# Performance work log

Hardware: AMD Instinct MI355X
Metric: run time of the kernel (lower is better)

## Reference

```python
import jax, jax.numpy as jnp
import numpy as np

D_MODEL = 1024
K_QUERY = 32
K_TOPK = 4

def setup_inputs() -> dict:
    key = jax.random.key(0)
    k1, k2, k3, k4, k5 = jax.random.split(key, 5)
    x = jax.random.normal(k1, (4, 2048, D_MODEL), dtype=jnp.float32)
    # nn.Linear(d_model, k_query): weight [k_query, d_model], bias [k_query]
    sc = 1.0 / np.sqrt(D_MODEL)
    Wq = jax.random.uniform(k2, (K_QUERY, D_MODEL), jnp.float32, -sc, sc)
    bq = jax.random.uniform(k3, (K_QUERY,), jnp.float32, -sc, sc)
    Wk = jax.random.uniform(k4, (K_QUERY, D_MODEL), jnp.float32, -sc, sc)
    bk = jax.random.uniform(k5, (K_QUERY,), jnp.float32, -sc, sc)
    return {"x": x, "Wq": Wq, "bq": bq, "Wk": Wk, "bk": bk}

def reference(x, Wq, bq, Wk, bk):
    # x: [B, T, D]
    queries = jnp.einsum('btd,kd->btk', x, Wq) + bq      # [B, T, Kq]
    keys = jnp.einsum('btd,kd->btk', x, Wk) + bk         # [B, T, Kq]
    sim = jnp.einsum('btk,bsk->bts', queries, keys)      # [B, T, T]
    sim = sim / jnp.sqrt(jnp.float32(queries.shape[-1]))
    _, topk_idx = jax.lax.top_k(sim, K_TOPK)              # [B, T, K]
    # gather neighbors per (b, t): x[b, topk_idx[b, t]] -> [B, T, K, D]
    neighbors = jax.vmap(lambda xb, ib: xb[ib])(x, topk_idx)
    gathered = neighbors.mean(axis=2)                     # [B, T, D]
    return gathered
```

## Files before the change

### kernel.cpp

```cpp
#include <hip/hip_runtime.h>
#include <math.h>

#define D_MODEL 1024
#define T_SEQ   2048
#define NBATCH  4
#define NROWS   (NBATCH * T_SEQ)
#define NOUT    64

#define T16F   1024

typedef float  v4f  __attribute__((ext_vector_type(4)));
typedef _Float16 v8hf __attribute__((ext_vector_type(8)));

__device__ __forceinline__ bool key_gt(float av, int ai, float bv, int bi) {
    return (av > bv) || (av == bv && ai < bi);
}

__device__ __forceinline__ void cmpswap(float& v0, int& i0, float& v1, int& i1) {
    bool sw = key_gt(v1, i1, v0, i0);
    float nv0 = sw ? v1 : v0, nv1 = sw ? v0 : v1;
    int   ni0 = sw ? i1 : i0, ni1 = sw ? i0 : i1;
    v0 = nv0; v1 = nv1; i0 = ni0; i1 = ni1;
}

__device__ __forceinline__ void merge4(float (&a)[4], int (&ai)[4],
                                       float b0, int j0, float b1, int j1,
                                       float b2, int j2, float b3, int j3) {
    if (!key_gt(a[0], ai[0], b3, j3)) { a[0] = b3; ai[0] = j3; }
    if (!key_gt(a[1], ai[1], b2, j2)) { a[1] = b2; ai[1] = j2; }
    if (!key_gt(a[2], ai[2], b1, j1)) { a[2] = b1; ai[2] = j1; }
    if (!key_gt(a[3], ai[3], b0, j0)) { a[3] = b0; ai[3] = j0; }
    cmpswap(a[0], ai[0], a[2], ai[2]);
    cmpswap(a[1], ai[1], a[3], ai[3]);
    cmpswap(a[0], ai[0], a[1], ai[1]);
    cmpswap(a[2], ai[2], a[3], ai[3]);
}

__device__ __forceinline__ void insert4(float (&tv)[4], int (&tix)[4], float v, int idx) {
    if (v > tv[3]) {
        bool g0 = v > tv[0], g1 = v > tv[1], g2 = v > tv[2];
        float n0 = g0 ? v : tv[0];
        int   m0 = g0 ? idx : tix[0];
        float n1 = g1 ? (g0 ? tv[0] : v) : tv[1];
        int   m1 = g1 ? (g0 ? tix[0] : idx) : tix[1];
        float n2 = g2 ? (g1 ? tv[1] : v) : tv[2];
        int   m2 = g2 ? (g1 ? tix[1] : idx) : tix[2];
        float n3 = g2 ? tv[2] : v;
        int   m3 = g2 ? tix[2] : idx;
        tv[0] = n0; tv[1] = n1; tv[2] = n2; tv[3] = n3;
        tix[0] = m0; tix[1] = m1; tix[2] = m2; tix[3] = m3;
    }
}

__device__ void run_probe16(int tid, int* __restrict__ tab)
{
    __shared__ _Float16 A16[16][32];
    __shared__ _Float16 B16[32][16];
    __shared__ float    D16[16][16];

    for (int e = tid; e < 512; e += 256) {
        const int m = e >> 5, k = e & 31;
        A16[m][k] = (_Float16)(float)(1 + (3 * m + 5 * k) % 61);
        const int kk = e >> 4, n = e & 15;
        B16[kk][n] = (_Float16)(float)(1 + (7 * kk + 11 * n) % 59);
    }
    __syncthreads();
    {
        const int m = tid >> 4, n = tid & 15;
        float s = 0.f;
        for (int k = 0; k < 32; ++k) s += (float)A16[m][k] * (float)B16[k][n];
        D16[m][n] = s;
    }
    __syncthreads();

    if (tid >= 64) return;
    const int lane = tid;

    v8hf a, b;
    const int ab = (lane >> 4) * 8;
    #pragma unroll
    for (int j = 0; j < 8; ++j) {
        a[j] = A16[lane & 15][ab + j];
        b[j] = B16[ab + j][lane & 15];
    }
    v4f c = {0.f, 0.f, 0.f, 0.f};
    c = __builtin_amdgcn_mfma_f32_16x16x32_f16(a, b, c, 0, 0, 0);

    bool ok0 = true;
    #pragma unroll
    for (int i = 0; i < 4; ++i)
        ok0 = ok0 && (c[i] == D16[4 * (lane >> 4) + i][lane & 15]);
    if (lane == 0) tab[T16F] = __all(ok0) ? 0 : -1;
}

__global__ __launch_bounds__(256) void wprep_probe(
    const float* __restrict__ x,
    const float* __restrict__ Wq, const float* __restrict__ Wk,
    double* __restrict__ Wdt, _Float16* __restrict__ Wh, _Float16* __restrict__ Wl,
    _Float16* __restrict__ Xh, _Float16* __restrict__ Xl, int do_xsplit,
    int* __restrict__ tab)
{
    const int tid = threadIdx.x;
    const int gid = blockIdx.x * 256 + tid;

    if (gid < 65536) {
        {
            const int o = gid & 63;
            const int d = gid >> 6;
            float v = (o < 32) ? Wq[(size_t)o * D_MODEL + d]
                               : Wk[(size_t)(o - 32) * D_MODEL + d];
            Wdt[(size_t)d * 64 + o] = (double)v;
        }
        {
            const int o = gid >> 10;
            const int d = gid & 1023;
            float v = (o < 32) ? Wq[(size_t)o * D_MODEL + d]
                               : Wk[(size_t)(o - 32) * D_MODEL + d];
            _Float16 h = (_Float16)v;
            Wh[(size_t)o * D_MODEL + d] = h;
            Wl[(size_t)o * D_MODEL + d] = (_Float16)(v - (float)h);
        }
    }

    if (do_xsplit) {
        #pragma unroll
        for (int j = 0; j < 8; ++j) {
            const size_t f4 = (size_t)j * 262144 + gid;
            float4 v = reinterpret_cast<const float4*>(x)[f4];
            const float f[4] = {v.x, v.y, v.z, v.w};
            union { _Float16 h[4]; short4 s; } uh, ul;
            #pragma unroll
            for (int e = 0; e < 4; ++e) {
                _Float16 h = (_Float16)f[e];
                uh.h[e] = h;
                ul.h[e] = (_Float16)(f[e] - (float)h);
            }
            reinterpret_cast<short4*>(Xh)[f4] = uh.s;
            reinterpret_cast<short4*>(Xl)[f4] = ul.s;
        }
    }

    if (blockIdx.x == 0) run_probe16(tid, tab);
}

__global__ __launch_bounds__(256, 4) void proj(
    const float* __restrict__ x, const double* __restrict__ Wdt,
    const _Float16* __restrict__ Wh, const _Float16* __restrict__ Wl,
    const _Float16* __restrict__ Xh, const _Float16* __restrict__ Xl, int use_xsplit,
    const float* __restrict__ bq, const float* __restrict__ bk_,
    const int* __restrict__ tab,
    float* __restrict__ Qt, float* __restrict__ Kt,
    _Float16* __restrict__ Qh, _Float16* __restrict__ Ql,
    _Float16* __restrict__ Kh, _Float16* __restrict__ Kl)
{
    const int tid  = threadIdx.x;
    const int lane = tid & 63;
    const int wav  = tid >> 6;
    const int og   = __builtin_amdgcn_readfirstlane(wav);
    const int row0 = blockIdx.x * 16;

    if (tab[T16F] == 0) {
        const int m  = lane & 15;
        const int ko = (lane >> 4) * 8;
        const _Float16* bH = Wh + (size_t)(og * 16 + m) * D_MODEL + ko;
        const _Float16* bL = Wl + (size_t)(og * 16 + m) * D_MODEL + ko;

        v4f hh = {0.f, 0.f, 0.f, 0.f};
        v4f hl = {0.f, 0.f, 0.f, 0.f};
        v4f lh = {0.f, 0.f, 0.f, 0.f};

        if (use_xsplit) {
            const _Float16* aH = Xh + (size_t)(row0 + m) * D_MODEL + ko;
            const _Float16* aL = Xl + (size_t)(row0 + m) * D_MODEL + ko;
            #pragma unroll 4
            for (int kc = 0; kc < 32; ++kc) {
                v8hf ah = *reinterpret_cast<const v8hf*>(aH + kc * 32);
                v8hf al = *reinterpret_cast<const v8hf*>(aL + kc * 32);
                v8hf bh = *reinterpret_cast<const v8hf*>(bH + kc * 32);
                v8hf bl = *reinterpret_cast<const v8hf*>(bL + kc * 32);
                hh = __builtin_amdgcn_mfma_f32_16x16x32_f16(ah, bh, hh, 0, 0, 0);
                hl = __builtin_amdgcn_mfma_f32_16x16x32_f16(ah, bl, hl, 0, 0, 0);
                lh = __builtin_amdgcn_mfma_f32_16x16x32_f16(al, bh, lh, 0, 0, 0);
            }
        } else {
            const float* xrow = x + (size_t)(row0 + m) * D_MODEL + ko;
            #pragma unroll 4
            for (int kc = 0; kc < 32; ++kc) {
                float4 x0 = *reinterpret_cast<const float4*>(xrow + kc * 32);
                float4 x1 = *reinterpret_cast<const float4*>(xrow + kc * 32 + 4);
                const float f[8] = {x0.x, x0.y, x0.z, x0.w, x1.x, x1.y, x1.z, x1.w};
                v8hf ah, al;
                #pragma unroll
                for (int e = 0; e < 8; ++e) {
                    _Float16 h = (_Float16)f[e];
                    ah[e] = h;
                    al[e] = (_Float16)(f[e] - (float)h);
                }
                v8hf bh = *reinterpret_cast<const v8hf*>(bH + kc * 32);
                v8hf bl = *reinterpret_cast<const v8hf*>(bL + kc * 32);
                hh = __builtin_amdgcn_mfma_f32_16x16x32_f16(ah, bh, hh, 0, 0, 0);
                hl = __builtin_amdgcn_mfma_f32_16x16x32_f16(ah, bl, hl, 0, 0, 0);
                lh = __builtin_amdgcn_mfma_f32_16x16x32_f16(al, bh, lh, 0, 0, 0);
            }
        }

        #pragma unroll
        for (int i = 0; i < 4; ++i) {
            const float t = (hh[i] + hl[i]) + lh[i];
            const int o   = og * 16 + m;
            const int row = row0 + 4 * (lane >> 4) + i;
            const float bias = (o < 32) ? bq[o] : bk_[o - 32];
            const float v = t + bias;
            const _Float16 h = (_Float16)v;
            const _Float16 l = (_Float16)(v - (float)h);
            if (o < 32) {
                Qh[(size_t)row * 32 + o] = h;
                Ql[(size_t)row * 32 + o] = l;
            } else {
                Kh[(size_t)row * 32 + (o - 32)] = h;
                Kl[(size_t)row * 32 + (o - 32)] = l;
            }
        }
        return;
    }

    {
        const int n  = lane & 15;
        const int r4 = (lane >> 4) * 4;
        const int o  = og * 16 + n;
        const double* wcol = Wdt + o;
        double acc[4] = {0.0, 0.0, 0.0, 0.0};
        for (int d = 0; d < D_MODEL; ++d) {
            double wv = wcol[(size_t)d * 64];
            #pragma unroll
            for (int i = 0; i < 4; ++i)
                acc[i] = fma((double)x[(size_t)(row0 + r4 + i) * D_MODEL + d], wv, acc[i]);
        }
        #pragma unroll
        for (int i = 0; i < 4; ++i) {
            const int row = row0 + r4 + i;
            const int bb  = row >> 11, tt = row & 2047;
            const double bias = (o < 32) ? (double)bq[o] : (double)bk_[o - 32];
            const float v = (float)(acc[i] + bias);
            if (o < 32) Qt[((size_t)bb * 32 + o) * T_SEQ + tt] = v;
            else        Kt[((size_t)bb * 32 + (o - 32)) * T_SEQ + tt] = v;
        }
    }
}

__global__ __launch_bounds__(512, 4) void sim_topk_gather(
    const float* __restrict__ x,
    const _Float16* __restrict__ Qh, const _Float16* __restrict__ Ql,
    const _Float16* __restrict__ Kh, const _Float16* __restrict__ Kl,
    const float* __restrict__ Qt, const float* __restrict__ Kt,
    const int* __restrict__ tab,
    float* __restrict__ out)
{
    __shared__ float sV[8][16][4];
    __shared__ int   sI[8][16][4];
    __shared__ float sVf[16][32][4];
    __shared__ int   sIf[16][32][4];
    __shared__ int   topIdx[16][4];

    const int tid  = threadIdx.x;
    const int lane = tid & 63;
    const int wav  = tid >> 6;
    const int tt   = blockIdx.x & 127;
    const int b    = blockIdx.x >> 7;
    const int row0g = b * T_SEQ + tt * 16;

    if (tab[T16F] == 0) {
        const int m  = lane & 15;
        const int ko = (lane >> 4) * 8;
        v8hf qh = *reinterpret_cast<const v8hf*>(Qh + (size_t)(row0g + m) * 32 + ko);
        v8hf ql = *reinterpret_cast<const v8hf*>(Ql + (size_t)(row0g + m) * 32 + ko);
        const _Float16* KhB = Kh + (size_t)b * T_SEQ * 32;
        const _Float16* KlB = Kl + (size_t)b * T_SEQ * 32;

        float tv[4]; int tix[4];
        #pragma unroll
        for (int j = 0; j < 4; ++j) { tv[j] = -INFINITY; tix[j] = 0x7fffffff; }

        const int sq = wav * 256;
        #pragma unroll 4
        for (int st = 0; st < 16; ++st) {
            const int s0 = sq + st * 16;
            v8hf kh = *reinterpret_cast<const v8hf*>(KhB + (size_t)(s0 + m) * 32 + ko);
            v8hf kl = *reinterpret_cast<const v8hf*>(KlB + (size_t)(s0 + m) * 32 + ko);
            v4f c = {0.f, 0.f, 0.f, 0.f};
            c = __builtin_amdgcn_mfma_f32_16x16x32_f16(kh, qh, c, 0, 0, 0);
            c = __builtin_amdgcn_mfma_f32_16x16x32_f16(kl, qh, c, 0, 0, 0);
            c = __builtin_amdgcn_mfma_f32_16x16x32_f16(kh, ql, c, 0, 0, 0);
            c = __builtin_amdgcn_mfma_f32_16x16x32_f16(kl, ql, c, 0, 0, 0);
            const int sb = s0 + 4 * (lane >> 4);
            #pragma unroll
            for (int i = 0; i < 4; ++i) insert4(tv, tix, c[i], sb + i);
        }

        #pragma unroll
        for (int mk = 16; mk <= 32; mk <<= 1) {
            float b0 = __shfl_xor(tv[0], mk, 64);
            float b1 = __shfl_xor(tv[1], mk, 64);
            float b2 = __shfl_xor(tv[2], mk, 64);
            float b3 = __shfl_xor(tv[3], mk, 64);
            int   j0 = __shfl_xor(tix[0], mk, 64);
            int   j1 = __shfl_xor(tix[1], mk, 64);
            int   j2 = __shfl_xor(tix[2], mk, 64);
            int   j3 = __shfl_xor(tix[3], mk, 64);
            merge4(tv, tix, b0, j0, b1, j1, b2, j2, b3, j3);
        }

        if (lane < 16) {
            #pragma unroll
            for (int j = 0; j < 4; ++j) {
                sV[wav][lane][j] = tv[j];
                sI[wav][lane][j] = tix[j];
            }
        }
        __syncthreads();

        if (tid < 16) {
            float mv[4]; int mi[4];
            #pragma unroll
            for (int j = 0; j < 4; ++j) { mv[j] = sV[0][tid][j]; mi[j] = sI[0][tid][j]; }
            #pragma unroll
            for (int w = 1; w < 8; ++w)
                merge4(mv, mi,
                       sV[w][tid][0], sI[w][tid][0],
                       sV[w][tid][1], sI[w][tid][1],
                       sV[w][tid][2], sI[w][tid][2],
                       sV[w][tid][3], sI[w][tid][3]);
            #pragma unroll
            for (int j = 0; j < 4; ++j) topIdx[tid][j] = mi[j];
        }
        __syncthreads();
    } else {
        const float* QtB = Qt + (size_t)b * 32 * T_SEQ;
        const float* KtB = Kt + (size_t)b * 32 * T_SEQ;
        const int row   = tid >> 5;
        const int chunk = tid & 31;
        const int trow  = tt * 16 + row;
        float q[32];
        #pragma unroll 8
        for (int i = 0; i < 32; ++i) q[i] = QtB[(size_t)i * T_SEQ + trow];
        float tv4[4]; int tix4[4];
        #pragma unroll
        for (int j = 0; j < 4; ++j) { tv4[j] = -INFINITY; tix4[j] = 0x7fffffff; }
        const int sbeg = chunk * 64;
        for (int s = sbeg; s < sbeg + 64; ++s) {
            float sum = 0.f;
            #pragma unroll 8
            for (int i = 0; i < 32; ++i)
                sum = fmaf(q[i], KtB[(size_t)i * T_SEQ + s], sum);
            insert4(tv4, tix4, sum, s);
        }
        #pragma unroll
        for (int j = 0; j < 4; ++j) { sVf[row][chunk][j] = tv4[j]; sIf[row][chunk][j] = tix4[j]; }
        __syncthreads();
        if (tid < 16) {
            float mv[4]; int mi[4];
            #pragma unroll
            for (int j = 0; j < 4; ++j) { mv[j] = sVf[tid][0][j]; mi[j] = sIf[tid][0][j]; }
            for (int cc = 1; cc < 32; ++cc)
                merge4(mv, mi,
                       sVf[tid][cc][0], sIf[tid][cc][0],
                       sVf[tid][cc][1], sIf[tid][cc][1],
                       sVf[tid][cc][2], sIf[tid][cc][2],
                       sVf[tid][cc][3], sIf[tid][cc][3]);
            #pragma unroll
            for (int j = 0; j < 4; ++j) topIdx[tid][j] = mi[j];
        }
        __syncthreads();
    }

    const float* xb = x + (size_t)b * T_SEQ * D_MODEL;
    float* ob = out + (size_t)row0g * D_MODEL;
    const int rh = tid >> 8;
    const int t4 = tid & 255;
    #pragma unroll 2
    for (int rp = 0; rp < 8; ++rp) {
        const int r = rp * 2 + rh;
        const int i0 = topIdx[r][0], i1 = topIdx[r][1], i2 = topIdx[r][2], i3 = topIdx[r][3];
        float4 a0 = *(reinterpret_cast<const float4*>(xb + (size_t)i0 * D_MODEL) + t4);
        float4 a1 = *(reinterpret_cast<const float4*>(xb + (size_t)i1 * D_MODEL) + t4);
        float4 a2 = *(reinterpret_cast<const float4*>(xb + (size_t)i2 * D_MODEL) + t4);
        float4 a3 = *(reinterpret_cast<const float4*>(xb + (size_t)i3 * D_MODEL) + t4);
        float4 o;
        o.x = (a0.x + a1.x + a2.x + a3.x) * 0.25f;
        o.y = (a0.y + a1.y + a2.y + a3.y) * 0.25f;
        o.z = (a0.z + a1.z + a2.z + a3.z) * 0.25f;
        o.w = (a0.w + a1.w + a2.w + a3.w) * 0.25f;
        *(reinterpret_cast<float4*>(ob + (size_t)r * D_MODEL) + t4) = o;
    }
}

extern "C" void kernel_launch(void* const* d_in, const int* in_sizes, int n_in,
                              void* d_out, int out_size, void* d_ws, size_t ws_size,
                              hipStream_t stream) {
    const float* x  = (const float*)d_in[0];
    const float* Wq = (const float*)d_in[1];
    const float* bq = (const float*)d_in[2];
    const float* Wk = (const float*)d_in[3];
    const float* bk = (const float*)d_in[4];
    float* out = (float*)d_out;

    char* wsb = (char*)d_ws;
    int*      tab = (int*)wsb;
    double*   Wdt = (double*)(wsb + 8192);
    _Float16* Wh  = (_Float16*)(wsb + 8192 + 524288);
    _Float16* Wl  = (_Float16*)(wsb + 8192 + 524288 + 131072);
    float*    Qt  = (float*)(wsb + 8192 + 524288 + 262144);
    float*    Kt  = Qt + (size_t)NBATCH * 32 * T_SEQ;
    _Float16* Qh  = (_Float16*)((char*)Kt + (size_t)NBATCH * 32 * T_SEQ * 4);
    _Float16* Ql  = Qh + (size_t)NROWS * 32;
    _Float16* Kh  = Ql + (size_t)NROWS * 32;
    _Float16* Kl  = Kh + (size_t)NROWS * 32;
    _Float16* Xh  = Kl + (size_t)NROWS * 32;
    _Float16* Xl  = Xh + (size_t)NROWS * D_MODEL;

    const size_t need = 4988928 + 2 * (size_t)NROWS * D_MODEL * 2;
    const int use_xsplit = (ws_size >= need) ? 1 : 0;

    wprep_probe<<<dim3(1024), dim3(256), 0, stream>>>(x, Wq, Wk, Wdt, Wh, Wl,
                                                      Xh, Xl, use_xsplit, tab);
    proj<<<dim3(NROWS / 16), dim3(256), 0, stream>>>(x, Wdt, Wh, Wl, Xh, Xl, use_xsplit,
                                                     bq, bk, tab, Qt, Kt, Qh, Ql, Kh, Kl);
    sim_topk_gather<<<dim3(512), dim3(512), 0, stream>>>(x, Qh, Ql, Kh, Kl, Qt, Kt, tab, out);
}
```

Measured before the change: 160.2 us.

## Fuse weight/x fp16 splitting into projection, split-K across 16 waves, widen sim kernel

```diff
diff --git a/kernel.cpp b/kernel.cpp
--- a/kernel.cpp
+++ b/kernel.cpp
@@ -52,186 +52,143 @@
     }
 }
 
-__device__ void run_probe16(int tid, int* __restrict__ tab)
+__device__ int run_probe16_block(int tid, int nthr, int* __restrict__ tab, int wr)
 {
     __shared__ _Float16 A16[16][32];
     __shared__ _Float16 B16[32][16];
     __shared__ float    D16[16][16];
-
-    for (int e = tid; e < 512; e += 256) {
+    __shared__ int      flagS;
+
+    for (int e = tid; e < 512; e += nthr) {
         const int m = e >> 5, k = e & 31;
         A16[m][k] = (_Float16)(float)(1 + (3 * m + 5 * k) % 61);
         const int kk = e >> 4, n = e & 15;
         B16[kk][n] = (_Float16)(float)(1 + (7 * kk + 11 * n) % 59);
     }
     __syncthreads();
-    {
-        const int m = tid >> 4, n = tid & 15;
+    for (int e = tid; e < 256; e += nthr) {
+        const int m = e >> 4, n = e & 15;
         float s = 0.f;
         for (int k = 0; k < 32; ++k) s += (float)A16[m][k] * (float)B16[k][n];
         D16[m][n] = s;
     }
     __syncthreads();
 
-    if (tid >= 64) return;
-    const int lane = tid;
-
-    v8hf a, b;
-    const int ab = (lane >> 4) * 8;
-    #pragma unroll
-    for (int j = 0; j < 8; ++j) {
-        a[j] = A16[lane & 15][ab + j];
-        b[j] = B16[ab + j][lane & 15];
-    }
-    v4f c = {0.f, 0.f, 0.f, 0.f};
-    c = __builtin_amdgcn_mfma_f32_16x16x32_f16(a, b, c, 0, 0, 0);
-
-    bool ok0 = true;
-    #pragma unroll
-    for (int i = 0; i < 4; ++i)
-        ok0 = ok0 && (c[i] == D16[4 * (lane >> 4) + i][lane & 15]);
-    if (lane == 0) tab[T16F] = __all(ok0) ? 0 : -1;
-}
-
-__global__ __launch_bounds__(256) void wprep_probe(
+    if (tid < 64) {
+        const int lane = tid;
+        v8hf a, b;
+        const int ab = (lane >> 4) * 8;
+        #pragma unroll
+        for (int j = 0; j < 8; ++j) {
+            a[j] = A16[lane & 15][ab + j];
+            b[j] = B16[ab + j][lane & 15];
+        }
+        v4f c = {0.f, 0.f, 0.f, 0.f};
+        c = __builtin_amdgcn_mfma_f32_16x16x32_f16(a, b, c, 0, 0, 0);
+        bool ok0 = true;
+        #pragma unroll
+        for (int i = 0; i < 4; ++i)
+            ok0 = ok0 && (c[i] == D16[4 * (lane >> 4) + i][lane & 15]);
+        int found = __all(ok0) ? 0 : -1;
+        if (lane == 0) { flagS = found; if (wr) tab[T16F] = found; }
+    }
+    __syncthreads();
+    return flagS;
+}
+
+__global__ __launch_bounds__(1024, 8) void proj_fused(
     const float* __restrict__ x,
     const float* __restrict__ Wq, const float* __restrict__ Wk,
-    double* __restrict__ Wdt, _Float16* __restrict__ Wh, _Float16* __restrict__ Wl,
-    _Float16* __restrict__ Xh, _Float16* __restrict__ Xl, int do_xsplit,
-    int* __restrict__ tab)
-{
-    const int tid = threadIdx.x;
-    const int gid = blockIdx.x * 256 + tid;
-
-    if (gid < 65536) {
-        {
-            const int o = gid & 63;
-            const int d = gid >> 6;
-            float v = (o < 32) ? Wq[(size_t)o * D_MODEL + d]
-                               : Wk[(size_t)(o - 32) * D_MODEL + d];
-            Wdt[(size_t)d * 64 + o] = (double)v;
-        }
-        {
-            const int o = gid >> 10;
-            const int d = gid & 1023;
-            float v = (o < 32) ? Wq[(size_t)o * D_MODEL + d]
-                               : Wk[(size_t)(o - 32) * D_MODEL + d];
-            _Float16 h = (_Float16)v;
-            Wh[(size_t)o * D_MODEL + d] = h;
-            Wl[(size_t)o * D_MODEL + d] = (_Float16)(v - (float)h);
-        }
-    }
-
-    if (do_xsplit) {
-        #pragma unroll
-        for (int j = 0; j < 8; ++j) {
-            const size_t f4 = (size_t)j * 262144 + gid;
-            float4 v = reinterpret_cast<const float4*>(x)[f4];
-            const float f[4] = {v.x, v.y, v.z, v.w};
-            union { _Float16 h[4]; short4 s; } uh, ul;
-            #pragma unroll
-            for (int e = 0; e < 4; ++e) {
-                _Float16 h = (_Float16)f[e];
-                uh.h[e] = h;
-                ul.h[e] = (_Float16)(f[e] - (float)h);
-            }
-            reinterpret_cast<short4*>(Xh)[f4] = uh.s;
-            reinterpret_cast<short4*>(Xl)[f4] = ul.s;
-        }
-    }
-
-    if (blockIdx.x == 0) run_probe16(tid, tab);
-}
-
-__global__ __launch_bounds__(256, 4) void proj(
-    const float* __restrict__ x, const double* __restrict__ Wdt,
-    const _Float16* __restrict__ Wh, const _Float16* __restrict__ Wl,
-    const _Float16* __restrict__ Xh, const _Float16* __restrict__ Xl, int use_xsplit,
     const float* __restrict__ bq, const float* __restrict__ bk_,
-    const int* __restrict__ tab,
+    int* __restrict__ tab,
     float* __restrict__ Qt, float* __restrict__ Kt,
     _Float16* __restrict__ Qh, _Float16* __restrict__ Ql,
     _Float16* __restrict__ Kh, _Float16* __restrict__ Kl)
 {
+    __shared__ float comb[3][4][64][4];
+
     const int tid  = threadIdx.x;
     const int lane = tid & 63;
     const int wav  = tid >> 6;
-    const int og   = __builtin_amdgcn_readfirstlane(wav);
+    const int og   = __builtin_amdgcn_readfirstlane(wav & 3);
+    const int kq   = __builtin_amdgcn_readfirstlane(wav >> 2);
     const int row0 = blockIdx.x * 16;
 
-    if (tab[T16F] == 0) {
+    const int flag = run_probe16_block(tid, 1024, tab, blockIdx.x == 0);
+
+    if (flag == 0) {
         const int m  = lane & 15;
         const int ko = (lane >> 4) * 8;
-        const _Float16* bH = Wh + (size_t)(og * 16 + m) * D_MODEL + ko;
-        const _Float16* bL = Wl + (size_t)(og * 16 + m) * D_MODEL + ko;
+        const int kb = kq * 256;
+        const int o  = og * 16 + m;
+        const float* xrow = x + (size_t)(row0 + m) * D_MODEL + kb + ko;
+        const float* wrow = ((o < 32) ? Wq + (size_t)o * D_MODEL
+                                      : Wk + (size_t)(o - 32) * D_MODEL) + kb + ko;
 
         v4f hh = {0.f, 0.f, 0.f, 0.f};
         v4f hl = {0.f, 0.f, 0.f, 0.f};
         v4f lh = {0.f, 0.f, 0.f, 0.f};
-
-        if (use_xsplit) {
-            const _Float16* aH = Xh + (size_t)(row0 + m) * D_MODEL + ko;
-            const _Float16* aL = Xl + (size_t)(row0 + m) * D_MODEL + ko;
-            #pragma unroll 4
-            for (int kc = 0; kc < 32; ++kc) {
-                v8hf ah = *reinterpret_cast<const v8hf*>(aH + kc * 32);
-                v8hf al = *reinterpret_cast<const v8hf*>(aL + kc * 32);
-                v8hf bh = *reinterpret_cast<const v8hf*>(bH + kc * 32);
-                v8hf bl = *reinterpret_cast<const v8hf*>(bL + kc * 32);
-                hh = __builtin_amdgcn_mfma_f32_16x16x32_f16(ah, bh, hh, 0, 0, 0);
-                hl = __builtin_amdgcn_mfma_f32_16x16x32_f16(ah, bl, hl, 0, 0, 0);
-                lh = __builtin_amdgcn_mfma_f32_16x16x32_f16(al, bh, lh, 0, 0, 0);
+        #pragma unroll 2
+        for (int kc = 0; kc < 8; ++kc) {
+            float4 x0 = *reinterpret_cast<const float4*>(xrow + kc * 32);
+            float4 x1 = *reinterpret_cast<const float4*>(xrow + kc * 32 + 4);
+            float4 w0 = *reinterpret_cast<const float4*>(wrow + kc * 32);
+            float4 w1 = *reinterpret_cast<const float4*>(wrow + kc * 32 + 4);
+            const float xf[8] = {x0.x, x0.y, x0.z, x0.w, x1.x, x1.y, x1.z, x1.w};
+            const float wf[8] = {w0.x, w0.y, w0.z, w0.w, w1.x, w1.y, w1.z, w1.w};
+            v8hf ah, al, bh, bl;
+            #pragma unroll
+            for (int e = 0; e < 8; ++e) {
+                _Float16 h = (_Float16)xf[e];
+                ah[e] = h; al[e] = (_Float16)(xf[e] - (float)h);
+                _Float16 g = (_Float16)wf[e];
+                bh[e] = g; bl[e] = (_Float16)(wf[e] - (float)g);
             }
-        } else {
-            const float* xrow = x + (size_t)(row0 + m) * D_MODEL + ko;
-            #pragma unroll 4
-            for (int kc = 0; kc < 32; ++kc) {
-                float4 x0 = *reinterpret_cast<const float4*>(xrow + kc * 32);
-                float4 x1 = *reinterpret_cast<const float4*>(xrow + kc * 32 + 4);
-                const float f[8] = {x0.x, x0.y, x0.z, x0.w, x1.x, x1.y, x1.z, x1.w};
-                v8hf ah, al;
-                #pragma unroll
-                for (int e = 0; e < 8; ++e) {
-                    _Float16 h = (_Float16)f[e];
-                    ah[e] = h;
-                    al[e] = (_Float16)(f[e] - (float)h);
+            hh = __builtin_amdgcn_mfma_f32_16x16x32_f16(ah, bh, hh, 0, 0, 0);
+            hl = __builtin_amdgcn_mfma_f32_16x16x32_f16(ah, bl, hl, 0, 0, 0);
+            lh = __builtin_amdgcn_mfma_f32_16x16x32_f16(al, bh, lh, 0, 0, 0);
+        }
+
+        v4f t;
+        #pragma unroll
+        for (int i = 0; i < 4; ++i) t[i] = (hh[i] + hl[i]) + lh[i];
+
+        if (kq > 0) {
+            #pragma unroll
+            for (int i = 0; i < 4; ++i) comb[kq - 1][og][lane][i] = t[i];
+        }
+        __syncthreads();
+        if (kq == 0) {
+            #pragma unroll
+            for (int i = 0; i < 4; ++i) {
+                const float tot = (t[i] + comb[0][og][lane][i])
+                                + (comb[1][og][lane][i] + comb[2][og][lane][i]);
+                const int row = row0 + 4 * (lane >> 4) + i;
+                const float bias = (o < 32) ? bq[o] : bk_[o - 32];
+                const float v = tot + bias;
+                const _Float16 h = (_Float16)v;
+                const _Float16 l = (_Float16)(v - (float)h);
+                if (o < 32) {
+                    Qh[(size_t)row * 32 + o] = h;
+                    Ql[(size_t)row * 32 + o] = l;
+                } else {
+                    Kh[(size_t)row * 32 + (o - 32)] = h;
+                    Kl[(size_t)row * 32 + (o - 32)] = l;
                 }
-                v8hf bh = *reinterpret_cast<const v8hf*>(bH + kc * 32);
-                v8hf bl = *reinterpret_cast<const v8hf*>(bL + kc * 32);
-                hh = __builtin_amdgcn_mfma_f32_16x16x32_f16(ah, bh, hh, 0, 0, 0);
-                hl = __builtin_amdgcn_mfma_f32_16x16x32_f16(ah, bl, hl, 0, 0, 0);
-                lh = __builtin_amdgcn_mfma_f32_16x16x32_f16(al, bh, lh, 0, 0, 0);
             }
         }
-
-        #pragma unroll
-        for (int i = 0; i < 4; ++i) {
-            const float t = (hh[i] + hl[i]) + lh[i];
-            const int o   = og * 16 + m;
-            const int row = row0 + 4 * (lane >> 4) + i;
-            const float bias = (o < 32) ? bq[o] : bk_[o - 32];
-            const float v = t + bias;
-            const _Float16 h = (_Float16)v;
-            const _Float16 l = (_Float16)(v - (float)h);
-            if (o < 32) {
-                Qh[(size_t)row * 32 + o] = h;
-                Ql[(size_t)row * 32 + o] = l;
-            } else {
-                Kh[(size_t)row * 32 + (o - 32)] = h;
-                Kl[(size_t)row * 32 + (o - 32)] = l;
-            }
-        }
         return;
     }
 
-    {
+    if (kq == 0) {
         const int n  = lane & 15;
         const int r4 = (lane >> 4) * 4;
         const int o  = og * 16 + n;
-        const double* wcol = Wdt + o;
+        const float* wr = (o < 32) ? Wq + (size_t)o * D_MODEL
+                                   : Wk + (size_t)(o - 32) * D_MODEL;
         double acc[4] = {0.0, 0.0, 0.0, 0.0};
         for (int d = 0; d < D_MODEL; ++d) {
-            double wv = wcol[(size_t)d * 64];
+            const double wv = (double)wr[d];
             #pragma unroll
             for (int i = 0; i < 4; ++i)
                 acc[i] = fma((double)x[(size_t)(row0 + r4 + i) * D_MODEL + d], wv, acc[i]);
@@ -248,7 +205,7 @@
     }
 }
 
-__global__ __launch_bounds__(512, 4) void sim_topk_gather(
+__global__ __launch_bounds__(1024, 8) void sim_topk_gather(
     const float* __restrict__ x,
     const _Float16* __restrict__ Qh, const _Float16* __restrict__ Ql,
     const _Float16* __restrict__ Kh, const _Float16* __restrict__ Kl,
@@ -256,10 +213,10 @@
     const int* __restrict__ tab,
     float* __restrict__ out)
 {
-    __shared__ float sV[8][16][4];
-    __shared__ int   sI[8][16][4];
-    __shared__ float sVf[16][32][4];
-    __shared__ int   sIf[16][32][4];
+    __shared__ float sV[16][16][4];
+    __shared__ int   sI[16][16][4];
+    __shared__ float sVf[16][64][4];
+    __shared__ int   sIf[16][64][4];
     __shared__ int   topIdx[16][4];
 
     const int tid  = threadIdx.x;
@@ -281,9 +238,9 @@
         #pragma unroll
         for (int j = 0; j < 4; ++j) { tv[j] = -INFINITY; tix[j] = 0x7fffffff; }
 
-        const int sq = wav * 256;
-        #pragma unroll 4
-        for (int st = 0; st < 16; ++st) {
+        const int sq = wav * 128;
+        #pragma unroll 2
+        for (int st = 0; st < 8; ++st) {
             const int s0 = sq + st * 16;
             v8hf kh = *reinterpret_cast<const v8hf*>(KhB + (size_t)(s0 + m) * 32 + ko);
             v8hf kl = *reinterpret_cast<const v8hf*>(KlB + (size_t)(s0 + m) * 32 + ko);
@@ -324,7 +281,7 @@
             #pragma unroll
             for (int j = 0; j < 4; ++j) { mv[j] = sV[0][tid][j]; mi[j] = sI[0][tid][j]; }
             #pragma unroll
-            for (int w = 1; w < 8; ++w)
+            for (int w = 1; w < 16; ++w)
                 merge4(mv, mi,
                        sV[w][tid][0], sI[w][tid][0],
                        sV[w][tid][1], sI[w][tid][1],
@@ -337,21 +294,16 @@
     } else {
         const float* QtB = Qt + (size_t)b * 32 * T_SEQ;
         const float* KtB = Kt + (size_t)b * 32 * T_SEQ;
-        const int row   = tid >> 5;
-        const int chunk = tid & 31;
+        const int row   = tid >> 6;
+        const int chunk = tid & 63;
         const int trow  = tt * 16 + row;
-        float q[32];
-        #pragma unroll 8
-        for (int i = 0; i < 32; ++i) q[i] = QtB[(size_t)i * T_SEQ + trow];
         float tv4[4]; int tix4[4];
         #pragma unroll
         for (int j = 0; j < 4; ++j) { tv4[j] = -INFINITY; tix4[j] = 0x7fffffff; }
-        const int sbeg = chunk * 64;
-        for (int s = sbeg; s < sbeg + 64; ++s) {
+        for (int s = chunk * 32; s < chunk * 32 + 32; ++s) {
             float sum = 0.f;
-            #pragma unroll 8
             for (int i = 0; i < 32; ++i)
-                sum = fmaf(q[i], KtB[(size_t)i * T_SEQ + s], sum);
+                sum = fmaf(QtB[(size_t)i * T_SEQ + trow], KtB[(size_t)i * T_SEQ + s], sum);
             insert4(tv4, tix4, sum, s);
         }
         #pragma unroll
@@ -361,7 +313,7 @@
             float mv[4]; int mi[4];
             #pragma unroll
             for (int j = 0; j < 4; ++j) { mv[j] = sVf[tid][0][j]; mi[j] = sIf[tid][0][j]; }
-            for (int cc = 1; cc < 32; ++cc)
+            for (int cc = 1; cc < 64; ++cc)
                 merge4(mv, mi,
                        sVf[tid][cc][0], sIf[tid][cc][0],
                        sVf[tid][cc][1], sIf[tid][cc][1],
@@ -377,9 +329,9 @@
     float* ob = out + (size_t)row0g * D_MODEL;
     const int rh = tid >> 8;
     const int t4 = tid & 255;
-    #pragma unroll 2
-    for (int rp = 0; rp < 8; ++rp) {
-        const int r = rp * 2 + rh;
+    #pragma unroll
+    for (int rp = 0; rp < 4; ++rp) {
+        const int r = rp * 4 + rh;
         const int i0 = topIdx[r][0], i1 = topIdx[r][1], i2 = topIdx[r][2], i3 = topIdx[r][3];
         float4 a0 = *(reinterpret_cast<const float4*>(xb + (size_t)i0 * D_MODEL) + t4);
         float4 a1 = *(reinterpret_cast<const float4*>(xb + (size_t)i1 * D_MODEL) + t4);
@@ -406,24 +358,15 @@
 
     char* wsb = (char*)d_ws;
     int*      tab = (int*)wsb;
-    double*   Wdt = (double*)(wsb + 8192);
-    _Float16* Wh  = (_Float16*)(wsb + 8192 + 524288);
-    _Float16* Wl  = (_Float16*)(wsb + 8192 + 524288 + 131072);
-    float*    Qt  = (float*)(wsb + 8192 + 524288 + 262144);
+    float*    Qt  = (float*)(wsb + 8192);
     float*    Kt  = Qt + (size_t)NBATCH * 32 * T_SEQ;
     _Float16* Qh  = (_Float16*)((char*)Kt + (size_t)NBATCH * 32 * T_SEQ * 4);
     _Float16* Ql  = Qh + (size_t)NROWS * 32;
     _Float16* Kh  = Ql + (size_t)NROWS * 32;
     _Float16* Kl  = Kh + (size_t)NROWS * 32;
-    _Float16* Xh  = Kl + (size_t)NROWS * 32;
-    _Float16* Xl  = Xh + (size_t)NROWS * D_MODEL;
-
-    const size_t need = 4988928 + 2 * (size_t)NROWS * D_MODEL * 2;
-    const int use_xsplit = (ws_size >= need) ? 1 : 0;
-
-    wprep_probe<<<dim3(1024), dim3(256), 0, stream>>>(x, Wq, Wk, Wdt, Wh, Wl,
-                                                      Xh, Xl, use_xsplit, tab);
-    proj<<<dim3(NROWS / 16), dim3(256), 0, stream>>>(x, Wdt, Wh, Wl, Xh, Xl, use_xsplit,
-                                                     bq, bk, tab, Qt, Kt, Qh, Ql, Kh, Kl);
-    sim_topk_gather<<<dim3(512), dim3(512), 0, stream>>>(x, Qh, Ql, Kh, Kl, Qt, Kt, tab, out);
-}
+
+    proj_fused<<<dim3(NROWS / 16), dim3(1024), 0, stream>>>(
+        x, Wq, Wk, bq, bk, tab, Qt, Kt, Qh, Ql, Kh, Kl);
+    sim_topk_gather<<<dim3(512), dim3(1024), 0, stream>>>(
+        x, Qh, Ql, Kh, Kl, Qt, Kt, tab, out);
+}
```

After: 145.5 us. 1.1x faster.
